# Optimization experiments

Hardware: AMD Instinct MI355X
Metric: run time of the kernel (lower is better)

The kernel has to match this reference:

```python
import jax, jax.numpy as jnp
import numpy as np

B, C, O, K, H, W = 32, 256, 256, 7, 31, 31


def _unfold(x, k):
    """Extract kxk sliding windows (stride 1, no padding, no dilation).

    x: [B, C, H, W] -> patches [B, C, k, k, Ho, Wo]
    """
    _, _, h, w = x.shape
    ho, wo = h - k + 1, w - k + 1
    # fixed small loop over k*k window offsets (k=7 -> 49 cheap slices)
    rows = []
    for i in range(k):
        cols = [x[:, :, i:i + ho, j:j + wo] for j in range(k)]
        rows.append(jnp.stack(cols, axis=2))  # [B, C, k, Ho, Wo]
    return jnp.stack(rows, axis=2)  # [B, C, k, k, Ho, Wo]


def setup_inputs() -> dict:
    key = jax.random.key(0)
    k1, k2, k3, k4 = jax.random.split(key, 4)
    x = jax.random.normal(k1, (B, C, H, W), dtype=jnp.float32)
    kernel = jax.random.normal(k2, (B, C, K, K), dtype=jnp.float32)
    weight = jax.random.normal(k3, (O, C, K, K), dtype=jnp.float32) * 0.02
    bias = jax.random.normal(k4, (O,), dtype=jnp.float32) * 0.02
    return {"x": x, "kernel": kernel, "weight": weight, "bias": bias}


def reference(x, kernel, weight, bias):
    k = weight.shape[-1]
    patches = _unfold(x, k)  # [B, C, k, k, Ho, Wo]
    # fused: (patches * kernel[..., None, None]) contracted with weight
    # torch: einsum('ijklmn,ojkl->iomn', patches * kernel_view, weight)
    out = jnp.einsum('bcklhw,bckl,ockl->bohw', patches, kernel, weight)
    out = out + bias[None, :, None, None]
    return out
```

## Files before the change

### kernel.cpp

```cpp
#include <hip/hip_runtime.h>
#include <hip/hip_bf16.h>

typedef __attribute__((ext_vector_type(8)))  short short8;
typedef __attribute__((ext_vector_type(4)))  float floatx4;
typedef __attribute__((ext_vector_type(16))) float floatx16;

#define BB 32
#define CC 256
#define OO 256
#define KS 7
#define HH 31
#define WW 31
#define HO 25
#define PP 625
#define SS 49

#define SLAB_PITCH 40
#define SLAB_ROWS  341
#define P_TILE 96
#define NPX 7
#define KP 36

#define WT4_ELEMS  ((size_t)SS * 8 * 2 * CC * 16)
#define WT4_BYTES  (WT4_ELEMS * 2)

static __device__ __forceinline__ unsigned pk2(float lo, float hi) {
    float2 f; f.x = lo; f.y = hi;
    __hip_bfloat162 h = __float22bfloat162_rn(f);
    unsigned r;
    __builtin_memcpy(&r, &h, sizeof(r));
    return r;
}
static __device__ __forceinline__ float bflo(unsigned u) {
    return __builtin_bit_cast(float, u << 16);
}
static __device__ __forceinline__ float bfhi(unsigned u) {
    return __builtin_bit_cast(float, u & 0xffff0000u);
}

static __device__ __forceinline__ uint4 modpack(uint4 wv, float4 k0, float4 k1) {
    float p0 = bflo(wv.x) * k0.x, p1 = bfhi(wv.x) * k0.y;
    float p2 = bflo(wv.y) * k0.z, p3 = bfhi(wv.y) * k0.w;
    float p4 = bflo(wv.z) * k1.x, p5 = bfhi(wv.z) * k1.y;
    float p6 = bflo(wv.w) * k1.z, p7 = bfhi(wv.w) * k1.w;
    uint4 r;
    r.x = pk2(p0, p1); r.y = pk2(p2, p3); r.z = pk2(p4, p5); r.w = pk2(p6, p7);
    return r;
}

__global__ __launch_bounds__(256) void repack_w(const float* __restrict__ w,
                                                unsigned short* __restrict__ wt4) {
    const int bid = blockIdx.x;
    const int s = bid >> 3, cb = bid & 7;
    const int o = threadIdx.x;
    const float* src = w + ((size_t)o * CC + cb * 32) * SS + s;
    float v[32];
#pragma unroll
    for (int ci = 0; ci < 32; ++ci) v[ci] = src[(size_t)ci * SS];
#pragma unroll
    for (int kh = 0; kh < 2; ++kh) {
        unsigned short* dst = wt4 + ((size_t)bid * 2 + kh) * (CC * 16) + o * 16;
        uint4 p0, p1;
        p0.x = pk2(v[kh*16+0], v[kh*16+1]);  p0.y = pk2(v[kh*16+2], v[kh*16+3]);
        p0.z = pk2(v[kh*16+4], v[kh*16+5]);  p0.w = pk2(v[kh*16+6], v[kh*16+7]);
        p1.x = pk2(v[kh*16+8], v[kh*16+9]);  p1.y = pk2(v[kh*16+10], v[kh*16+11]);
        p1.z = pk2(v[kh*16+12], v[kh*16+13]); p1.w = pk2(v[kh*16+14], v[kh*16+15]);
        *(uint4*)(dst)     = p0;
        *(uint4*)(dst + 8) = p1;
    }
}

__global__ __launch_bounds__(256, 3) void dwconv_fused(
        const float* __restrict__ x, const unsigned short* __restrict__ wt4,
        const float* __restrict__ kern, const float* __restrict__ bias,
        float* __restrict__ out) {
    __shared__ unsigned short slab[SLAB_ROWS * SLAB_PITCH];
    __shared__ float klds[SS * KP];

    const int tid = threadIdx.x;
    const int id = blockIdx.x;
    const int q = id >> 3, r = id & 7;
    const int oy = r >> 2;
    const int m = q * 4 + (r & 3);
    const int b = m / NPX, px = m - (m / NPX) * NPX;

    const int p0 = px * P_TILE;
    const int h0 = p0 / HO;
    const int pmax = (p0 + P_TILE - 1 < PP - 1) ? p0 + P_TILE - 1 : PP - 1;
    const int rows = pmax / HO - h0 + 7;
    const int npos = rows * WW;

    const int lane = tid & 63, wid = tid >> 6;
    const int l32 = lane & 31, half = lane >> 5;

    int bOff[3];
#pragma unroll
    for (int ph = 0; ph < 3; ++ph) {
        int p = p0 + ph * 32 + l32;
        if (p > PP - 1) p = PP - 1;
        int h = p / HO, ww_ = p - h * HO;
        bOff[ph] = ((h - h0) * WW + ww_) * SLAB_PITCH + half * 8;
    }

    const unsigned short* wbase = wt4
        + (size_t)(oy * 128 + wid * 32 + l32) * 16 + half * 8;

    floatx16 acc[3];
#pragma unroll
    for (int ph = 0; ph < 3; ++ph)
#pragma unroll
        for (int rr = 0; rr < 16; ++rr) acc[ph][rr] = 0.f;

    for (int cb = 0; cb < 8; ++cb) {
        __syncthreads();
        {
            const float* xsrc = x + ((size_t)(b * CC + cb * 32 + wid * 8)) * (HH * WW)
                                  + h0 * WW;
#pragma unroll
            for (int it = 0; it < 6; ++it) {
                int pos = lane + it * 64;
                if (pos < npos) {
                    float v[8];
#pragma unroll
                    for (int j = 0; j < 8; ++j) v[j] = xsrc[j * (HH * WW) + pos];
                    uint4 pkt;
                    pkt.x = pk2(v[0], v[1]); pkt.y = pk2(v[2], v[3]);
                    pkt.z = pk2(v[4], v[5]); pkt.w = pk2(v[6], v[7]);
                    *(uint4*)(slab + pos * SLAB_PITCH + wid * 8) = pkt;
                }
            }
        }
        {
            const float* ksrc = kern + ((size_t)(b * CC + cb * 32)) * SS;
#pragma unroll
            for (int it = 0; it < 7; ++it) {
                int f = tid + it * 256;
                if (f < 32 * SS) {
                    int c = f / SS, s = f - c * SS;
                    klds[s * KP + c] = ksrc[f];
                }
            }
        }
        __syncthreads();

        const unsigned short* aptr = wbase + (size_t)cb * 8192;

        uint4 wa0 = *(const uint4*)(aptr);
        uint4 wa1 = *(const uint4*)(aptr + 4096);

        int kk = 0, ll = 0;
        for (int si = 0; si < SS; ++si) {
            uint4 wn0, wn1;
            if (si + 1 < SS) {
                aptr += 65536;
                wn0 = *(const uint4*)(aptr);
                wn1 = *(const uint4*)(aptr + 4096);
            } else {
                wn0 = wa0; wn1 = wa1;
            }

            const float* kp = klds + si * KP;
            float4 k0a = *(const float4*)(kp + half * 8);
            float4 k0b = *(const float4*)(kp + half * 8 + 4);
            float4 k1a = *(const float4*)(kp + 16 + half * 8);
            float4 k1b = *(const float4*)(kp + 16 + half * 8 + 4);

            const unsigned short* slabS = slab + (kk * WW + ll) * SLAB_PITCH;
            short8 sb00 = *(const short8*)(slabS + bOff[0]);
            short8 sb01 = *(const short8*)(slabS + bOff[0] + 16);
            short8 sb10 = *(const short8*)(slabS + bOff[1]);
            short8 sb11 = *(const short8*)(slabS + bOff[1] + 16);
            short8 sb20 = *(const short8*)(slabS + bOff[2]);
            short8 sb21 = *(const short8*)(slabS + bOff[2] + 16);

            short8 a0 = __builtin_bit_cast(short8, modpack(wa0, k0a, k0b));
            short8 a1 = __builtin_bit_cast(short8, modpack(wa1, k1a, k1b));

            acc[0] = __builtin_amdgcn_mfma_f32_32x32x16_bf16(a0, sb00, acc[0], 0, 0, 0);
            acc[1] = __builtin_amdgcn_mfma_f32_32x32x16_bf16(a0, sb10, acc[1], 0, 0, 0);
            acc[2] = __builtin_amdgcn_mfma_f32_32x32x16_bf16(a0, sb20, acc[2], 0, 0, 0);
            acc[0] = __builtin_amdgcn_mfma_f32_32x32x16_bf16(a1, sb01, acc[0], 0, 0, 0);
            acc[1] = __builtin_amdgcn_mfma_f32_32x32x16_bf16(a1, sb11, acc[1], 0, 0, 0);
            acc[2] = __builtin_amdgcn_mfma_f32_32x32x16_bf16(a1, sb21, acc[2], 0, 0, 0);

            wa0 = wn0; wa1 = wn1;
            if (++ll == KS) { ll = 0; ++kk; }
        }
    }

    const int ow0 = oy * 128 + wid * 32;
#pragma unroll
    for (int c = 0; c < 4; ++c) {
        const int ob = ow0 + c * 8 + 4 * half;
        const float4 bv = *(const float4*)(bias + ob);
#pragma unroll
        for (int ph = 0; ph < 3; ++ph) {
            const int p = p0 + ph * 32 + l32;
            if (p < PP) {
                out[((size_t)(b * OO + ob + 0)) * PP + p] = acc[ph][4*c+0] + bv.x;
                out[((size_t)(b * OO + ob + 1)) * PP + p] = acc[ph][4*c+1] + bv.y;
                out[((size_t)(b * OO + ob + 2)) * PP + p] = acc[ph][4*c+2] + bv.z;
                out[((size_t)(b * OO + ob + 3)) * PP + p] = acc[ph][4*c+3] + bv.w;
            }
        }
    }
}

__global__ __launch_bounds__(256) void dwconv_naive(
        const float* __restrict__ x, const float* __restrict__ kern,
        const float* __restrict__ w, const float* __restrict__ bias,
        float* __restrict__ out) {
    const int idx = blockIdx.x * 256 + threadIdx.x;
    if (idx >= BB * OO * PP) return;
    const int p = idx % PP;
    const int o = (idx / PP) % OO;
    const int b = idx / (PP * OO);
    const int h = p / HO;
    const int wq = p - h * HO;
    float acc = 0.f;
    for (int c = 0; c < CC; ++c) {
        const float* xp = x + ((size_t)(b * CC + c)) * (HH * WW) + h * WW + wq;
        const float* kp = kern + ((size_t)b * CC + c) * SS;
        const float* wp = w + ((size_t)o * CC + c) * SS;
#pragma unroll
        for (int s = 0; s < SS; ++s) {
            const int kk = s / KS;
            const int ll = s - kk * KS;
            acc += xp[kk * WW + ll] * kp[s] * wp[s];
        }
    }
    out[idx] = acc + bias[o];
}

extern "C" void kernel_launch(void* const* d_in, const int* in_sizes, int n_in,
                              void* d_out, int out_size, void* d_ws, size_t ws_size,
                              hipStream_t stream) {
    const float* x    = (const float*)d_in[0];
    const float* kern = (const float*)d_in[1];
    const float* w    = (const float*)d_in[2];
    const float* bias = (const float*)d_in[3];
    float* out = (float*)d_out;

    if (ws_size >= WT4_BYTES) {
        unsigned short* wt4 = (unsigned short*)d_ws;
        repack_w<<<dim3(SS * 8), dim3(256), 0, stream>>>(w, wt4);
        dwconv_fused<<<dim3(448), dim3(256), 0, stream>>>(x, wt4, kern, bias, out);
    } else {
        const int total = BB * OO * PP;
        dwconv_naive<<<dim3((total + 255) / 256), dim3(256), 0, stream>>>(
            x, kern, w, bias, out);
    }
}
```

Measured before the change: 321.3 us.

## Switch to fp16 MFMA with packed half2 kernel modulation and smaller tiles

Moves the inputs, weights and per-batch kernel values from bf16 to fp16. The weight-times-kernel modulation now runs as packed half2 multiplies on values stored pre-packed in shared memory, instead of unpacking bf16 to fp32 and repacking. The pixel tile shrinks from 96 to 64 positions and the grid grows from 448 to 640 blocks with occupancy hint 4, which cuts per-block accumulators. Weight loads are now prefetched two steps ahead. fp16 gives more mantissa than bf16 but risks overflow or underflow in the modulated products, and smaller tiles mean more redundant slab loads.

```diff
diff --git a/kernel.cpp b/kernel.cpp
--- a/kernel.cpp
+++ b/kernel.cpp
@@ -1,7 +1,7 @@
 #include <hip/hip_runtime.h>
-#include <hip/hip_bf16.h>
-
-typedef __attribute__((ext_vector_type(8)))  short short8;
+#include <hip/hip_fp16.h>
+
+typedef _Float16 half8 __attribute__((ext_vector_type(8)));
 typedef __attribute__((ext_vector_type(4)))  float floatx4;
 typedef __attribute__((ext_vector_type(16))) float floatx16;
 
@@ -16,36 +16,33 @@
 #define SS 49
 
 #define SLAB_PITCH 40
-#define SLAB_ROWS  341
-#define P_TILE 96
-#define NPX 7
-#define KP 36
+#define SLAB_ROWS  310
+#define P_TILE 64
+#define NPX 10
+#define KPD 20
 
 #define WT4_ELEMS  ((size_t)SS * 8 * 2 * CC * 16)
 #define WT4_BYTES  (WT4_ELEMS * 2)
 
-static __device__ __forceinline__ unsigned pk2(float lo, float hi) {
-    float2 f; f.x = lo; f.y = hi;
-    __hip_bfloat162 h = __float22bfloat162_rn(f);
+static __device__ __forceinline__ unsigned pk2h(float lo, float hi) {
+    __half2 h = __floats2half2_rn(lo, hi);
     unsigned r;
     __builtin_memcpy(&r, &h, sizeof(r));
     return r;
 }
-static __device__ __forceinline__ float bflo(unsigned u) {
-    return __builtin_bit_cast(float, u << 16);
-}
-static __device__ __forceinline__ float bfhi(unsigned u) {
-    return __builtin_bit_cast(float, u & 0xffff0000u);
-}
-
-static __device__ __forceinline__ uint4 modpack(uint4 wv, float4 k0, float4 k1) {
-    float p0 = bflo(wv.x) * k0.x, p1 = bfhi(wv.x) * k0.y;
-    float p2 = bflo(wv.y) * k0.z, p3 = bfhi(wv.y) * k0.w;
-    float p4 = bflo(wv.z) * k1.x, p5 = bfhi(wv.z) * k1.y;
-    float p6 = bflo(wv.w) * k1.z, p7 = bfhi(wv.w) * k1.w;
+static __device__ __forceinline__ unsigned mulh2(unsigned a, unsigned b) {
+    __half2 x, y;
+    __builtin_memcpy(&x, &a, 4); __builtin_memcpy(&y, &b, 4);
+    __half2 r = __hmul2(x, y);
+    unsigned u;
+    __builtin_memcpy(&u, &r, 4);
+    return u;
+}
+static __device__ __forceinline__ half8 mod8(uint4 w, uint4 k) {
     uint4 r;
-    r.x = pk2(p0, p1); r.y = pk2(p2, p3); r.z = pk2(p4, p5); r.w = pk2(p6, p7);
-    return r;
+    r.x = mulh2(w.x, k.x); r.y = mulh2(w.y, k.y);
+    r.z = mulh2(w.z, k.z); r.w = mulh2(w.w, k.w);
+    return __builtin_bit_cast(half8, r);
 }
 
 __global__ __launch_bounds__(256) void repack_w(const float* __restrict__ w,
@@ -61,27 +58,26 @@
     for (int kh = 0; kh < 2; ++kh) {
         unsigned short* dst = wt4 + ((size_t)bid * 2 + kh) * (CC * 16) + o * 16;
         uint4 p0, p1;
-        p0.x = pk2(v[kh*16+0], v[kh*16+1]);  p0.y = pk2(v[kh*16+2], v[kh*16+3]);
-        p0.z = pk2(v[kh*16+4], v[kh*16+5]);  p0.w = pk2(v[kh*16+6], v[kh*16+7]);
-        p1.x = pk2(v[kh*16+8], v[kh*16+9]);  p1.y = pk2(v[kh*16+10], v[kh*16+11]);
-        p1.z = pk2(v[kh*16+12], v[kh*16+13]); p1.w = pk2(v[kh*16+14], v[kh*16+15]);
+        p0.x = pk2h(v[kh*16+0], v[kh*16+1]);  p0.y = pk2h(v[kh*16+2], v[kh*16+3]);
+        p0.z = pk2h(v[kh*16+4], v[kh*16+5]);  p0.w = pk2h(v[kh*16+6], v[kh*16+7]);
+        p1.x = pk2h(v[kh*16+8], v[kh*16+9]);  p1.y = pk2h(v[kh*16+10], v[kh*16+11]);
+        p1.z = pk2h(v[kh*16+12], v[kh*16+13]); p1.w = pk2h(v[kh*16+14], v[kh*16+15]);
         *(uint4*)(dst)     = p0;
         *(uint4*)(dst + 8) = p1;
     }
 }
 
-__global__ __launch_bounds__(256, 3) void dwconv_fused(
+__global__ __launch_bounds__(256, 4) void dwconv_fused(
         const float* __restrict__ x, const unsigned short* __restrict__ wt4,
         const float* __restrict__ kern, const float* __restrict__ bias,
         float* __restrict__ out) {
     __shared__ unsigned short slab[SLAB_ROWS * SLAB_PITCH];
-    __shared__ float klds[SS * KP];
+    __shared__ unsigned klds[SS * KPD];
 
     const int tid = threadIdx.x;
     const int id = blockIdx.x;
-    const int q = id >> 3, r = id & 7;
-    const int oy = r >> 2;
-    const int m = q * 4 + (r & 3);
+    const int oy = id & 1;
+    const int m = id >> 1;
     const int b = m / NPX, px = m - (m / NPX) * NPX;
 
     const int p0 = px * P_TILE;
@@ -93,9 +89,9 @@
     const int lane = tid & 63, wid = tid >> 6;
     const int l32 = lane & 31, half = lane >> 5;
 
-    int bOff[3];
-#pragma unroll
-    for (int ph = 0; ph < 3; ++ph) {
+    int bOff[2];
+#pragma unroll
+    for (int ph = 0; ph < 2; ++ph) {
         int p = p0 + ph * 32 + l32;
         if (p > PP - 1) p = PP - 1;
         int h = p / HO, ww_ = p - h * HO;
@@ -105,9 +101,9 @@
     const unsigned short* wbase = wt4
         + (size_t)(oy * 128 + wid * 32 + l32) * 16 + half * 8;
 
-    floatx16 acc[3];
-#pragma unroll
-    for (int ph = 0; ph < 3; ++ph)
+    floatx16 acc[2];
+#pragma unroll
+    for (int ph = 0; ph < 2; ++ph)
 #pragma unroll
         for (int rr = 0; rr < 16; ++rr) acc[ph][rr] = 0.f;
 
@@ -117,15 +113,15 @@
             const float* xsrc = x + ((size_t)(b * CC + cb * 32 + wid * 8)) * (HH * WW)
                                   + h0 * WW;
 #pragma unroll
-            for (int it = 0; it < 6; ++it) {
+            for (int it = 0; it < 5; ++it) {
                 int pos = lane + it * 64;
                 if (pos < npos) {
                     float v[8];
 #pragma unroll
                     for (int j = 0; j < 8; ++j) v[j] = xsrc[j * (HH * WW) + pos];
                     uint4 pkt;
-                    pkt.x = pk2(v[0], v[1]); pkt.y = pk2(v[2], v[3]);
-                    pkt.z = pk2(v[4], v[5]); pkt.w = pk2(v[6], v[7]);
+                    pkt.x = pk2h(v[0], v[1]); pkt.y = pk2h(v[2], v[3]);
+                    pkt.z = pk2h(v[4], v[5]); pkt.w = pk2h(v[6], v[7]);
                     *(uint4*)(slab + pos * SLAB_PITCH + wid * 8) = pkt;
                 }
             }
@@ -133,57 +129,54 @@
         {
             const float* ksrc = kern + ((size_t)(b * CC + cb * 32)) * SS;
 #pragma unroll
-            for (int it = 0; it < 7; ++it) {
+            for (int it = 0; it < 4; ++it) {
                 int f = tid + it * 256;
-                if (f < 32 * SS) {
-                    int c = f / SS, s = f - c * SS;
-                    klds[s * KP + c] = ksrc[f];
+                if (f < 16 * SS) {
+                    int s = f >> 4, pr = f & 15;
+                    float v0 = ksrc[(size_t)(pr * 2) * SS + s];
+                    float v1 = ksrc[(size_t)(pr * 2 + 1) * SS + s];
+                    klds[s * KPD + pr] = pk2h(v0, v1);
                 }
             }
         }
         __syncthreads();
 
         const unsigned short* aptr = wbase + (size_t)cb * 8192;
-
-        uint4 wa0 = *(const uint4*)(aptr);
-        uint4 wa1 = *(const uint4*)(aptr + 4096);
+        uint4 a0k0 = *(const uint4*)(aptr);
+        uint4 a0k1 = *(const uint4*)(aptr + 4096);
+        uint4 a1k0 = *(const uint4*)(aptr + 65536);
+        uint4 a1k1 = *(const uint4*)(aptr + 65536 + 4096);
 
         int kk = 0, ll = 0;
         for (int si = 0; si < SS; ++si) {
-            uint4 wn0, wn1;
-            if (si + 1 < SS) {
-                aptr += 65536;
-                wn0 = *(const uint4*)(aptr);
-                wn1 = *(const uint4*)(aptr + 4096);
+            uint4 n0, n1;
+            if (si + 2 < SS) {
+                const unsigned short* p2 = aptr + 2 * 65536;
+                n0 = *(const uint4*)(p2);
+                n1 = *(const uint4*)(p2 + 4096);
             } else {
-                wn0 = wa0; wn1 = wa1;
-            }
-
-            const float* kp = klds + si * KP;
-            float4 k0a = *(const float4*)(kp + half * 8);
-            float4 k0b = *(const float4*)(kp + half * 8 + 4);
-            float4 k1a = *(const float4*)(kp + 16 + half * 8);
-            float4 k1b = *(const float4*)(kp + 16 + half * 8 + 4);
+                n0 = a1k0; n1 = a1k1;
+            }
+
+            uint4 kv0 = *(const uint4*)(klds + si * KPD + half * 4);
+            uint4 kv1 = *(const uint4*)(klds + si * KPD + 8 + half * 4);
 
             const unsigned short* slabS = slab + (kk * WW + ll) * SLAB_PITCH;
-            short8 sb00 = *(const short8*)(slabS + bOff[0]);
-            short8 sb01 = *(const short8*)(slabS + bOff[0] + 16);
-            short8 sb10 = *(const short8*)(slabS + bOff[1]);
-            short8 sb11 = *(const short8*)(slabS + bOff[1] + 16);
-            short8 sb20 = *(const short8*)(slabS + bOff[2]);
-            short8 sb21 = *(const short8*)(slabS + bOff[2] + 16);
-
-            short8 a0 = __builtin_bit_cast(short8, modpack(wa0, k0a, k0b));
-            short8 a1 = __builtin_bit_cast(short8, modpack(wa1, k1a, k1b));
-
-            acc[0] = __builtin_amdgcn_mfma_f32_32x32x16_bf16(a0, sb00, acc[0], 0, 0, 0);
-            acc[1] = __builtin_amdgcn_mfma_f32_32x32x16_bf16(a0, sb10, acc[1], 0, 0, 0);
-            acc[2] = __builtin_amdgcn_mfma_f32_32x32x16_bf16(a0, sb20, acc[2], 0, 0, 0);
-            acc[0] = __builtin_amdgcn_mfma_f32_32x32x16_bf16(a1, sb01, acc[0], 0, 0, 0);
-            acc[1] = __builtin_amdgcn_mfma_f32_32x32x16_bf16(a1, sb11, acc[1], 0, 0, 0);
-            acc[2] = __builtin_amdgcn_mfma_f32_32x32x16_bf16(a1, sb21, acc[2], 0, 0, 0);
-
-            wa0 = wn0; wa1 = wn1;
+            half8 b00 = *(const half8*)(slabS + bOff[0]);
+            half8 b01 = *(const half8*)(slabS + bOff[0] + 16);
+            half8 b10 = *(const half8*)(slabS + bOff[1]);
+            half8 b11 = *(const half8*)(slabS + bOff[1] + 16);
+
+            half8 a0 = mod8(a0k0, kv0);
+            half8 a1 = mod8(a0k1, kv1);
+
+            acc[0] = __builtin_amdgcn_mfma_f32_32x32x16_f16(a0, b00, acc[0], 0, 0, 0);
+            acc[1] = __builtin_amdgcn_mfma_f32_32x32x16_f16(a0, b10, acc[1], 0, 0, 0);
+            acc[0] = __builtin_amdgcn_mfma_f32_32x32x16_f16(a1, b01, acc[0], 0, 0, 0);
+            acc[1] = __builtin_amdgcn_mfma_f32_32x32x16_f16(a1, b11, acc[1], 0, 0, 0);
+
+            a0k0 = a1k0; a0k1 = a1k1; a1k0 = n0; a1k1 = n1;
+            aptr += 65536;
             if (++ll == KS) { ll = 0; ++kk; }
         }
     }
@@ -194,7 +187,7 @@
         const int ob = ow0 + c * 8 + 4 * half;
         const float4 bv = *(const float4*)(bias + ob);
 #pragma unroll
-        for (int ph = 0; ph < 3; ++ph) {
+        for (int ph = 0; ph < 2; ++ph) {
             const int p = p0 + ph * 32 + l32;
             if (p < PP) {
                 out[((size_t)(b * OO + ob + 0)) * PP + p] = acc[ph][4*c+0] + bv.x;
@@ -244,7 +237,7 @@
     if (ws_size >= WT4_BYTES) {
         unsigned short* wt4 = (unsigned short*)d_ws;
         repack_w<<<dim3(SS * 8), dim3(256), 0, stream>>>(w, wt4);
-        dwconv_fused<<<dim3(448), dim3(256), 0, stream>>>(x, wt4, kern, bias, out);
+        dwconv_fused<<<dim3(640), dim3(256), 0, stream>>>(x, wt4, kern, bias, out);
     } else {
         const int total = BB * OO * PP;
         dwconv_naive<<<dim3((total + 255) / 256), dim3(256), 0, stream>>>(
```

After: 292.8 us. -8.9%, faster.
